# Kernel tuning notes

Hardware: AMD Instinct MI355X
Metric: run time of the kernel (lower is better)

Reference implementation:

```python
import jax, jax.numpy as jnp
import numpy as np


def setup_inputs() -> dict:
    key = jax.random.key(0)
    B, C, H, W = 8, 64, 64, 64
    x = jax.random.normal(key, (B, C, H, W), dtype=jnp.float32)
    return {"x": x}


def reference(x) -> jnp.ndarray:
    # x: (B, C, H, W). Spatial self-attention over N = H*W positions with
    # Q = K = V = flattened x, no scaling, no projections (the Conv2d in the
    # original __init__ is never used in forward).
    B, C, H, W = x.shape
    N = H * W
    f = x.reshape(B, C, N)  # (B, C, N)
    # att[b, n, m] = sum_c f[b, c, n] * f[b, c, m]  -> (B, N, N)
    att = jnp.einsum('bcn,bcm->bnm', f, f)
    att = jax.nn.softmax(att, axis=-1)
    # outp[b, c, n] = sum_m f[b, c, m] * att[b, n, m]^T  (f_x @ att)
    outp = jnp.einsum('bcm,bmn->bcn', f, att).reshape(B, C, H, W)
    return x + outp
```

## Files before the change

kernel.cpp:

```cpp
#include <hip/hip_runtime.h>

typedef short v8s __attribute__((ext_vector_type(8)));
typedef float v4f __attribute__((ext_vector_type(4)));

#define CC 64
#define NN 4096
#define NKT 32
#define LOG2E 1.44269504088896340736f

#define WS_FBF_T 0u
#define WS_FBF   4194304u
#define WS_G     8388608u
#define WS_MAXN  8519680u
#define WS_NEED  8519712u

__device__ __forceinline__ unsigned short f2bf_rne(float f) {
  unsigned int u = __builtin_bit_cast(unsigned int, f);
  u += 0x7FFFu + ((u >> 16) & 1u);
  return (unsigned short)(u >> 16);
}

__global__ __launch_bounds__(256) void prep_kernel(
    const float* __restrict__ x, unsigned short* __restrict__ fbf_t,
    unsigned short* __restrict__ fbf, float* __restrict__ g, int* __restrict__ maxn) {
  __shared__ unsigned short T[64 * 72];
  __shared__ float red[16][64];
  const int t = threadIdx.x;
  const int b = blockIdx.x & 7;
  const int n0 = (blockIdx.x >> 3) << 6;
  const int nn = (t & 15) << 2;
  float ps0 = 0.f, ps1 = 0.f, ps2 = 0.f, ps3 = 0.f;
#pragma unroll
  for (int j = 0; j < 4; ++j) {
    int c = (t >> 4) + j * 16;
    size_t gidx = ((size_t)(b * 64 + c) << 12) + (unsigned)(n0 + nn);
    float4 v = *(const float4*)(x + gidx);
    ushort4 w;
    w.x = f2bf_rne(v.x); w.y = f2bf_rne(v.y); w.z = f2bf_rne(v.z); w.w = f2bf_rne(v.w);
    *(ushort4*)(fbf + gidx) = w;
    T[(nn + 0) * 72 + c] = w.x;
    T[(nn + 1) * 72 + c] = w.y;
    T[(nn + 2) * 72 + c] = w.z;
    T[(nn + 3) * 72 + c] = w.w;
    ps0 += v.x * v.x; ps1 += v.y * v.y; ps2 += v.z * v.z; ps3 += v.w * v.w;
  }
  red[t >> 4][nn + 0] = ps0; red[t >> 4][nn + 1] = ps1;
  red[t >> 4][nn + 2] = ps2; red[t >> 4][nn + 3] = ps3;
  __syncthreads();
  if (t < 64) {
    float gs = 0.f;
#pragma unroll
    for (int i = 0; i < 16; ++i) gs += red[i][t];
    g[b * 4096 + n0 + t] = gs;
    float m = gs;
    m = fmaxf(m, __shfl_xor(m, 1, 64));
    m = fmaxf(m, __shfl_xor(m, 2, 64));
    m = fmaxf(m, __shfl_xor(m, 4, 64));
    m = fmaxf(m, __shfl_xor(m, 8, 64));
    m = fmaxf(m, __shfl_xor(m, 16, 64));
    m = fmaxf(m, __shfl_xor(m, 32, 64));
    if (t == 0) atomicMax(maxn + b, __float_as_int(m));
  }
#pragma unroll
  for (int i = 0; i < 2; ++i) {
    int idx = t + i * 256;
    int n = idx >> 3, cs = (idx & 7) << 3;
    *(v8s*)(fbf_t + (((size_t)b << 12) + (unsigned)(n0 + n)) * 64 + cs) =
        *(const v8s*)&T[n * 72 + cs];
  }
}

__global__ __launch_bounds__(512, 2) void chanattn_main(
    const float* __restrict__ x, const unsigned short* __restrict__ fbf_t,
    const unsigned short* __restrict__ fbf, const float* __restrict__ g,
    const int* __restrict__ maxn, float* __restrict__ out) {
  __shared__ __align__(16) unsigned char smem[56320];
  unsigned short* sKt = (unsigned short*)smem;
  unsigned short* sVc = (unsigned short*)(smem + 18432);
  unsigned short* sP  = (unsigned short*)(smem + 35840);

  const int tid = threadIdx.x;
  const int wave = tid >> 6, lane = tid & 63, quad = lane >> 4, l15 = lane & 15;
  const int qg = wave >> 2, kg = wave & 3;
  const int b = blockIdx.x & 7, qt = blockIdx.x >> 3;

  const unsigned short* fT = fbf_t + (((size_t)b << 12) << 6);
  const unsigned short* fV = fbf + ((size_t)b << 18);

  const int sKey = tid >> 3, sC = (tid & 7) << 3;
  const int vC = tid >> 4, vK = (tid & 15) << 3;

#pragma unroll
  for (int i = 0; i < 2; ++i) {
    int key = sKey + i * 64;
    *(v8s*)&sKt[key * 72 + sC] =
        *(const v8s*)&fT[((size_t)(qt * 128 + key)) * 64 + sC];
  }
  __syncthreads();
  v8s aqf[4][2];
#pragma unroll
  for (int mt = 0; mt < 4; ++mt)
#pragma unroll
    for (int cs = 0; cs < 2; ++cs)
      aqf[mt][cs] = *(const v8s*)&sKt[(qg * 64 + mt * 16 + l15) * 72 + cs * 32 + quad * 8];

  float msc[4][4];
  {
    const float gmax = __int_as_float(maxn[b]);
#pragma unroll
    for (int mt = 0; mt < 4; ++mt)
#pragma unroll
      for (int r = 0; r < 4; ++r) {
        int row = qt * 128 + qg * 64 + mt * 16 + quad * 4 + r;
        msc[mt][r] = __builtin_sqrtf(g[b * 4096 + row] * gmax) * LOG2E;
      }
  }
  __syncthreads();

  v8s pf[4];
#pragma unroll
  for (int i = 0; i < 2; ++i)
    pf[i] = *(const v8s*)&fT[((size_t)(sKey + i * 64)) * 64 + sC];
#pragma unroll
  for (int i = 0; i < 2; ++i)
    pf[2 + i] = *(const v8s*)&fV[(size_t)(vC + i * 32) * 4096 + vK];

  v4f oacc[4][4];
  float rsum[4][4];
#pragma unroll
  for (int mt = 0; mt < 4; ++mt)
#pragma unroll
    for (int r = 0; r < 4; ++r) {
      oacc[mt][r] = (v4f){0.f, 0.f, 0.f, 0.f};
      rsum[mt][r] = 0.f;
    }
  unsigned short* sPw = sP + wave * (32 * 40);

  for (int kt = 0; kt < NKT; ++kt) {
#pragma unroll
    for (int i = 0; i < 2; ++i)
      *(v8s*)&sKt[(sKey + i * 64) * 72 + sC] = pf[i];
#pragma unroll
    for (int i = 0; i < 2; ++i)
      *(v8s*)&sVc[(vC + i * 32) * 136 + vK] = pf[2 + i];
    __syncthreads();
    if (kt + 1 < NKT) {
      const int k0 = (kt + 1) * 128;
#pragma unroll
      for (int i = 0; i < 2; ++i)
        pf[i] = *(const v8s*)&fT[((size_t)(k0 + sKey + i * 64)) * 64 + sC];
#pragma unroll
      for (int i = 0; i < 2; ++i)
        pf[2 + i] = *(const v8s*)&fV[(size_t)(vC + i * 32) * 4096 + k0 + vK];
    }

    v4f sacc[4][2];
#pragma unroll
    for (int mt = 0; mt < 4; ++mt)
#pragma unroll
      for (int nt = 0; nt < 2; ++nt) sacc[mt][nt] = (v4f){0.f, 0.f, 0.f, 0.f};
#pragma unroll
    for (int nt = 0; nt < 2; ++nt)
#pragma unroll
      for (int cs = 0; cs < 2; ++cs) {
        v8s bK = *(const v8s*)&sKt[(kg * 32 + 2 * l15 + nt) * 72 + cs * 32 + quad * 8];
#pragma unroll
        for (int mt = 0; mt < 4; ++mt)
          sacc[mt][nt] =
              __builtin_amdgcn_mfma_f32_16x16x32_bf16(aqf[mt][cs], bK, sacc[mt][nt], 0, 0, 0);
      }

    unsigned int pk[4][4];
#pragma unroll
    for (int mt = 0; mt < 4; ++mt)
#pragma unroll
      for (int r = 0; r < 4; ++r) {
        float p0 = __builtin_amdgcn_exp2f(__builtin_fmaf(sacc[mt][0][r], LOG2E, -msc[mt][r]));
        float p1 = __builtin_amdgcn_exp2f(__builtin_fmaf(sacc[mt][1][r], LOG2E, -msc[mt][r]));
        rsum[mt][r] += p0 + p1;
        unsigned int u0 = __builtin_bit_cast(unsigned int, p0);
        unsigned int u1 = __builtin_bit_cast(unsigned int, p1);
        pk[mt][r] = (u1 & 0xFFFF0000u) | (u0 >> 16);
      }

    v8s bV[4];
#pragma unroll
    for (int ct = 0; ct < 4; ++ct)
      bV[ct] = *(const v8s*)&sVc[(ct * 16 + l15) * 136 + kg * 32 + quad * 8];
#pragma unroll
    for (int h = 0; h < 2; ++h) {
#pragma unroll
      for (int m2 = 0; m2 < 2; ++m2)
#pragma unroll
        for (int r = 0; r < 4; ++r)
          *(unsigned int*)&sPw[(m2 * 16 + quad * 4 + r) * 40 + 2 * l15] = pk[h * 2 + m2][r];
      asm volatile("s_waitcnt lgkmcnt(0)" ::: "memory");
      v8s aP[2];
#pragma unroll
      for (int m2 = 0; m2 < 2; ++m2)
        aP[m2] = *(const v8s*)&sPw[(m2 * 16 + l15) * 40 + quad * 8];
      asm volatile("s_waitcnt lgkmcnt(0)" ::: "memory");
#pragma unroll
      for (int m2 = 0; m2 < 2; ++m2)
#pragma unroll
        for (int ct = 0; ct < 4; ++ct)
          oacc[h * 2 + m2][ct] = __builtin_amdgcn_mfma_f32_16x16x32_bf16(
              aP[m2], bV[ct], oacc[h * 2 + m2][ct], 0, 0, 0);
    }
    __syncthreads();
  }

#pragma unroll
  for (int mt = 0; mt < 4; ++mt)
#pragma unroll
    for (int r = 0; r < 4; ++r) {
      float s = rsum[mt][r];
      s += __shfl_xor(s, 1, 64);
      s += __shfl_xor(s, 2, 64);
      s += __shfl_xor(s, 4, 64);
      s += __shfl_xor(s, 8, 64);
      rsum[mt][r] = s;
    }
  float* lred = (float*)(smem + 35840);
  if (l15 == 0) {
#pragma unroll
    for (int mt = 0; mt < 4; ++mt)
#pragma unroll
      for (int r = 0; r < 4; ++r)
        lred[(qg * 64 + mt * 16 + quad * 4 + r) * 4 + kg] = rsum[mt][r];
  }
  __syncthreads();
  float inv[4][4];
#pragma unroll
  for (int mt = 0; mt < 4; ++mt)
#pragma unroll
    for (int r = 0; r < 4; ++r) {
      const float4 lv = *(const float4*)&lred[(qg * 64 + mt * 16 + quad * 4 + r) * 4];
      inv[mt][r] = __builtin_amdgcn_rcpf(lv.x + lv.y + lv.z + lv.w);
    }

  float* Obuf = (float*)smem;
#pragma unroll
  for (int round = 0; round < 4; ++round) {
    if (kg == round) {
#pragma unroll
      for (int mt = 0; mt < 4; ++mt)
#pragma unroll
        for (int ct = 0; ct < 4; ++ct)
#pragma unroll
          for (int r = 0; r < 4; ++r) {
            float val = oacc[mt][ct][r] * inv[mt][r];
            float* p = &Obuf[(qg * 64 + ct * 16 + l15) * 68 + mt * 16 + quad * 4 + r];
            if (round == 0) *p = val; else *p += val;
          }
    }
    __syncthreads();
  }
#pragma unroll
  for (int j = 0; j < 4; ++j) {
    int idx = tid + j * 512;
    int qg2 = idx >> 10, c = (idx >> 4) & 63, q4 = idx & 15;
    const float4 o = *(const float4*)&Obuf[(qg2 * 64 + c) * 68 + q4 * 4];
    size_t gidx = ((size_t)(b * 64 + c) << 12) + (unsigned)(qt * 128 + qg2 * 64 + q4 * 4);
    const float4 xv = *(const float4*)(x + gidx);
    float4 rv;
    rv.x = xv.x + o.x; rv.y = xv.y + o.y; rv.z = xv.z + o.z; rv.w = xv.w + o.w;
    *(float4*)(out + gidx) = rv;
  }
}

__global__ __launch_bounds__(512) void
chanattn_fallback(const float* __restrict__ x, float* __restrict__ out) {
  __shared__ __align__(16) unsigned char smem[54272];
  unsigned short* sKt = (unsigned short*)smem;
  unsigned short* sVc = (unsigned short*)(smem + 18432);
  unsigned short* sP  = (unsigned short*)(smem + 35840);
  const int tid = threadIdx.x;
  const int wave = tid >> 6, lane = tid & 63, quad = lane >> 4, l15 = lane & 15;
  const int b = blockIdx.x & 7, qt = blockIdx.x >> 3;
  const float* fb = x + (size_t)b * (CC * NN);
  const int skey = tid & 127, sc0 = (tid >> 7) << 4;
  {
    float vq[16];
#pragma unroll
    for (int j = 0; j < 16; ++j) vq[j] = fb[(sc0 + j) * NN + qt * 128 + skey];
    unsigned short us[16];
#pragma unroll
    for (int j = 0; j < 16; ++j) us[j] = f2bf_rne(vq[j]);
#pragma unroll
    for (int h = 0; h < 2; ++h) {
      v8s t;
#pragma unroll
      for (int j = 0; j < 8; ++j) t[j] = (short)us[h * 8 + j];
      *(v8s*)&sKt[skey * 72 + sc0 + h * 8] = t;
    }
  }
  float vk[16];
#pragma unroll
  for (int j = 0; j < 16; ++j) vk[j] = fb[(sc0 + j) * NN + skey];
  __syncthreads();
  v8s aq[2];
#pragma unroll
  for (int cs = 0; cs < 2; ++cs)
    aq[cs] = *(const v8s*)&sKt[(wave * 16 + l15) * 72 + cs * 32 + quad * 8];
  __syncthreads();
  v4f oacc[4];
#pragma unroll
  for (int ct = 0; ct < 4; ++ct) oacc[ct] = (v4f){0.f, 0.f, 0.f, 0.f};
  float m_run[4], l_run[4];
#pragma unroll
  for (int r = 0; r < 4; ++r) { m_run[r] = -3.0e38f; l_run[r] = 0.f; }
  unsigned short* sPw = sP + wave * (16 * 72);
  for (int kt = 0; kt < 32; ++kt) {
    {
      unsigned short us[16];
#pragma unroll
      for (int j = 0; j < 16; ++j) us[j] = f2bf_rne(vk[j]);
#pragma unroll
      for (int h = 0; h < 2; ++h) {
        v8s t;
#pragma unroll
        for (int j = 0; j < 8; ++j) t[j] = (short)us[h * 8 + j];
        *(v8s*)&sKt[skey * 72 + sc0 + h * 8] = t;
      }
#pragma unroll
      for (int j = 0; j < 16; ++j) sVc[(sc0 + j) * 136 + skey] = us[j];
    }
    __syncthreads();
    if (kt + 1 < 32) {
      const int m0 = (kt + 1) * 128;
#pragma unroll
      for (int j = 0; j < 16; ++j) vk[j] = fb[(sc0 + j) * NN + m0 + skey];
    }
    v4f sacc[8];
#pragma unroll
    for (int t = 0; t < 8; ++t) {
      v4f acc = (v4f){0.f, 0.f, 0.f, 0.f};
#pragma unroll
      for (int cs = 0; cs < 2; ++cs) {
        v8s bf = *(const v8s*)&sKt[(t * 16 + l15) * 72 + cs * 32 + quad * 8];
        acc = __builtin_amdgcn_mfma_f32_16x16x32_bf16(aq[cs], bf, acc, 0, 0, 0);
      }
      sacc[t] = acc;
    }
    float alpha[4], msc[4], rsum[4];
#pragma unroll
    for (int r = 0; r < 4; ++r) {
      float mv = sacc[0][r];
#pragma unroll
      for (int t = 1; t < 8; ++t) mv = fmaxf(mv, sacc[t][r]);
      mv = fmaxf(mv, __shfl_xor(mv, 8, 64));
      mv = fmaxf(mv, __shfl_xor(mv, 4, 64));
      mv = fmaxf(mv, __shfl_xor(mv, 2, 64));
      mv = fmaxf(mv, __shfl_xor(mv, 1, 64));
      float mnew = fmaxf(m_run[r], mv);
      alpha[r] = __builtin_amdgcn_exp2f((m_run[r] - mnew) * LOG2E);
      m_run[r] = mnew;
      msc[r] = mnew * LOG2E;
      l_run[r] *= alpha[r];
      rsum[r] = 0.f;
    }
#pragma unroll
    for (int ct = 0; ct < 4; ++ct)
#pragma unroll
      for (int r = 0; r < 4; ++r) oacc[ct][r] *= alpha[r];
#pragma unroll
    for (int half = 0; half < 2; ++half) {
#pragma unroll
      for (int t = half * 4; t < half * 4 + 4; ++t)
#pragma unroll
        for (int r = 0; r < 4; ++r) {
          float p = __builtin_amdgcn_exp2f(__builtin_fmaf(sacc[t][r], LOG2E, -msc[r]));
          rsum[r] += p;
          sPw[(quad * 4 + r) * 72 + (t - half * 4) * 16 + l15] = f2bf_rne(p);
        }
      asm volatile("s_waitcnt lgkmcnt(0)" ::: "memory");
#pragma unroll
      for (int ms = 0; ms < 2; ++ms) {
        v8s af = *(const v8s*)&sPw[l15 * 72 + ms * 32 + quad * 8];
#pragma unroll
        for (int ct = 0; ct < 4; ++ct) {
          v8s bf = *(const v8s*)&sVc[(ct * 16 + l15) * 136 + (half * 2 + ms) * 32 + quad * 8];
          oacc[ct] = __builtin_amdgcn_mfma_f32_16x16x32_bf16(af, bf, oacc[ct], 0, 0, 0);
        }
      }
      asm volatile("s_waitcnt lgkmcnt(0)" ::: "memory");
    }
#pragma unroll
    for (int r = 0; r < 4; ++r) {
      float s = rsum[r];
      s += __shfl_xor(s, 8, 64);
      s += __shfl_xor(s, 4, 64);
      s += __shfl_xor(s, 2, 64);
      s += __shfl_xor(s, 1, 64);
      l_run[r] += s;
    }
    __syncthreads();
  }
  float inv[4];
#pragma unroll
  for (int r = 0; r < 4; ++r) inv[r] = __builtin_amdgcn_rcpf(l_run[r]);
  float* sOt = (float*)smem;
#pragma unroll
  for (int ct = 0; ct < 4; ++ct)
#pragma unroll
    for (int r = 0; r < 4; ++r)
      sOt[(ct * 16 + l15) * 132 + wave * 16 + quad * 4 + r] = oacc[ct][r] * inv[r];
  __syncthreads();
#pragma unroll
  for (int j = 0; j < 4; ++j) {
    int idx = tid + j * 512;
    int nv = idx & 31, c = idx >> 5;
    float4 o = *(const float4*)&sOt[c * 132 + nv * 4];
    size_t gaddr = (size_t)b * (CC * NN) + (size_t)c * NN + (size_t)(qt * 128 + nv * 4);
    float4 xv = *(const float4*)(x + gaddr);
    float4 res = make_float4(xv.x + o.x, xv.y + o.y, xv.z + o.z, xv.w + o.w);
    *(float4*)(out + gaddr) = res;
  }
}

extern "C" void kernel_launch(void* const* d_in, const int* in_sizes, int n_in,
                              void* d_out, int out_size, void* d_ws, size_t ws_size,
                              hipStream_t stream) {
  const float* xin = (const float*)d_in[0];
  float* out = (float*)d_out;
  if (ws_size >= (size_t)WS_NEED) {
    unsigned short* fbf_t = (unsigned short*)((char*)d_ws + WS_FBF_T);
    unsigned short* fbf = (unsigned short*)((char*)d_ws + WS_FBF);
    float* g = (float*)((char*)d_ws + WS_G);
    int* maxn = (int*)((char*)d_ws + WS_MAXN);
    hipMemsetAsync(maxn, 0, 8 * sizeof(int), stream);
    prep_kernel<<<dim3(512), dim3(256), 0, stream>>>(xin, fbf_t, fbf, g, maxn);
    chanattn_main<<<dim3(256), dim3(512), 0, stream>>>(xin, fbf_t, fbf, g, maxn, out);
  } else {
    chanattn_fallback<<<dim3(256), dim3(512), 0, stream>>>(xin, out);
  }
}
```

Baseline: 120.7 us.

## Transpose attention MFMAs so P stays in registers, drop LDS P roundtrip

The score MFMA is reordered to compute S^T (keys as rows, queries as columns), so each lane's exp outputs can be packed directly into the B operand of the PV MFMA with no per-wave LDS staging buffer for P. V is stored in LDS with a permuted column slot so its fragment order matches the register-packed P layout. The K/V tile loop now reads its fragments into registers before a barrier and then writes the next tile, which double-buffers through registers and frees shared memory. This removes LDS writes and reads plus waitcnt stalls per tile, but adds a second barrier per iteration and depends on the permuted-slot mapping being correct.

```diff
diff --git a/kernel.cpp b/kernel.cpp
--- a/kernel.cpp
+++ b/kernel.cpp
@@ -1,11 +1,9 @@
 #include <hip/hip_runtime.h>
 
 typedef short v8s __attribute__((ext_vector_type(8)));
+typedef short v4s __attribute__((ext_vector_type(4)));
 typedef float v4f __attribute__((ext_vector_type(4)));
 
-#define CC 64
-#define NN 4096
-#define NKT 32
 #define LOG2E 1.44269504088896340736f
 
 #define WS_FBF_T 0u
@@ -74,183 +72,183 @@
     const float* __restrict__ x, const unsigned short* __restrict__ fbf_t,
     const unsigned short* __restrict__ fbf, const float* __restrict__ g,
     const int* __restrict__ maxn, float* __restrict__ out) {
-  __shared__ __align__(16) unsigned char smem[56320];
+  __shared__ __align__(16) unsigned char smem[37888];
   unsigned short* sKt = (unsigned short*)smem;
   unsigned short* sVc = (unsigned short*)(smem + 18432);
-  unsigned short* sP  = (unsigned short*)(smem + 35840);
+  float* lred = (float*)(smem + 35840);
 
   const int tid = threadIdx.x;
   const int wave = tid >> 6, lane = tid & 63, quad = lane >> 4, l15 = lane & 15;
   const int qg = wave >> 2, kg = wave & 3;
   const int b = blockIdx.x & 7, qt = blockIdx.x >> 3;
 
-  const unsigned short* fT = fbf_t + (((size_t)b << 12) << 6);
+  const unsigned short* fT = fbf_t + ((size_t)b << 18);
   const unsigned short* fV = fbf + ((size_t)b << 18);
 
   const int sKey = tid >> 3, sC = (tid & 7) << 3;
   const int vC = tid >> 4, vK = (tid & 15) << 3;
-
-#pragma unroll
-  for (int i = 0; i < 2; ++i) {
-    int key = sKey + i * 64;
-    *(v8s*)&sKt[key * 72 + sC] =
-        *(const v8s*)&fT[((size_t)(qt * 128 + key)) * 64 + sC];
-  }
-  __syncthreads();
-  v8s aqf[4][2];
-#pragma unroll
-  for (int mt = 0; mt < 4; ++mt)
+  const int vSlot = (vK & ~31) + ((vK & 8) ? 16 : 0) + ((vK & 16) ? 4 : 0);
+
+#pragma unroll
+  for (int i = 0; i < 2; ++i)
+    *(v8s*)&sKt[(sKey + i * 64) * 72 + sC] =
+        *(const v8s*)&fT[(size_t)(qt * 128 + sKey + i * 64) * 64 + sC];
+
+  v8s pfk[2], pfv[2];
+#pragma unroll
+  for (int i = 0; i < 2; ++i)
+    pfk[i] = *(const v8s*)&fT[(size_t)(sKey + i * 64) * 64 + sC];
+#pragma unroll
+  for (int i = 0; i < 2; ++i)
+    pfv[i] = *(const v8s*)&fV[(size_t)(vC + i * 32) * 4096 + vK];
+
+  __syncthreads();
+  v8s bQ[4][2];
+#pragma unroll
+  for (int jq = 0; jq < 4; ++jq)
 #pragma unroll
     for (int cs = 0; cs < 2; ++cs)
-      aqf[mt][cs] = *(const v8s*)&sKt[(qg * 64 + mt * 16 + l15) * 72 + cs * 32 + quad * 8];
-
-  float msc[4][4];
+      bQ[jq][cs] = *(const v8s*)&sKt[(qg * 64 + jq * 16 + l15) * 72 + cs * 32 + quad * 8];
+
+  float msc[4];
   {
     const float gmax = __int_as_float(maxn[b]);
 #pragma unroll
-    for (int mt = 0; mt < 4; ++mt)
+    for (int jq = 0; jq < 4; ++jq) {
+      int row = qt * 128 + qg * 64 + jq * 16 + l15;
+      msc[jq] = __builtin_sqrtf(g[b * 4096 + row] * gmax) * LOG2E;
+    }
+  }
+  __syncthreads();
+
+#pragma unroll
+  for (int i = 0; i < 2; ++i)
+    *(v8s*)&sKt[(sKey + i * 64) * 72 + sC] = pfk[i];
+#pragma unroll
+  for (int i = 0; i < 2; ++i) {
+    v4s lo, hi;
+#pragma unroll
+    for (int j = 0; j < 4; ++j) { lo[j] = pfv[i][j]; hi[j] = pfv[i][j + 4]; }
+    *(v4s*)&sVc[(vC + i * 32) * 136 + vSlot] = lo;
+    *(v4s*)&sVc[(vC + i * 32) * 136 + vSlot + 8] = hi;
+  }
+
+  v4f oacc[4][4];
+  float rsum[4];
+#pragma unroll
+  for (int ct = 0; ct < 4; ++ct)
+#pragma unroll
+    for (int jq = 0; jq < 4; ++jq) oacc[ct][jq] = (v4f){0.f, 0.f, 0.f, 0.f};
+#pragma unroll
+  for (int jq = 0; jq < 4; ++jq) rsum[jq] = 0.f;
+
+  for (int kt = 0; kt < 32; ++kt) {
+    __syncthreads();
+
+    if (kt + 1 < 32) {
+      const int k0 = (kt + 1) * 128;
+#pragma unroll
+      for (int i = 0; i < 2; ++i)
+        pfk[i] = *(const v8s*)&fT[(size_t)(k0 + sKey + i * 64) * 64 + sC];
+#pragma unroll
+      for (int i = 0; i < 2; ++i)
+        pfv[i] = *(const v8s*)&fV[(size_t)(vC + i * 32) * 4096 + k0 + vK];
+    }
+
+    v8s aK[2][2];
+#pragma unroll
+    for (int t = 0; t < 2; ++t)
+#pragma unroll
+      for (int cs = 0; cs < 2; ++cs)
+        aK[t][cs] =
+            *(const v8s*)&sKt[(kg * 32 + t * 16 + l15) * 72 + cs * 32 + quad * 8];
+    v8s aV[4];
+#pragma unroll
+    for (int ct = 0; ct < 4; ++ct)
+      aV[ct] = *(const v8s*)&sVc[(ct * 16 + l15) * 136 + kg * 32 + quad * 8];
+
+    __syncthreads();
+
+    if (kt + 1 < 32) {
+#pragma unroll
+      for (int i = 0; i < 2; ++i)
+        *(v8s*)&sKt[(sKey + i * 64) * 72 + sC] = pfk[i];
+#pragma unroll
+      for (int i = 0; i < 2; ++i) {
+        v4s lo, hi;
+#pragma unroll
+        for (int j = 0; j < 4; ++j) { lo[j] = pfv[i][j]; hi[j] = pfv[i][j + 4]; }
+        *(v4s*)&sVc[(vC + i * 32) * 136 + vSlot] = lo;
+        *(v4s*)&sVc[(vC + i * 32) * 136 + vSlot + 8] = hi;
+      }
+    }
+
+#pragma unroll
+    for (int jq = 0; jq < 4; ++jq) {
+      v4f s0 = (v4f){0.f, 0.f, 0.f, 0.f};
+      v4f s1 = (v4f){0.f, 0.f, 0.f, 0.f};
+#pragma unroll
+      for (int cs = 0; cs < 2; ++cs) {
+        s0 = __builtin_amdgcn_mfma_f32_16x16x32_bf16(aK[0][cs], bQ[jq][cs], s0, 0, 0, 0);
+        s1 = __builtin_amdgcn_mfma_f32_16x16x32_bf16(aK[1][cs], bQ[jq][cs], s1, 0, 0, 0);
+      }
+      float p0[4], p1[4];
 #pragma unroll
       for (int r = 0; r < 4; ++r) {
-        int row = qt * 128 + qg * 64 + mt * 16 + quad * 4 + r;
-        msc[mt][r] = __builtin_sqrtf(g[b * 4096 + row] * gmax) * LOG2E;
-      }
-  }
-  __syncthreads();
-
-  v8s pf[4];
-#pragma unroll
-  for (int i = 0; i < 2; ++i)
-    pf[i] = *(const v8s*)&fT[((size_t)(sKey + i * 64)) * 64 + sC];
-#pragma unroll
-  for (int i = 0; i < 2; ++i)
-    pf[2 + i] = *(const v8s*)&fV[(size_t)(vC + i * 32) * 4096 + vK];
-
-  v4f oacc[4][4];
-  float rsum[4][4];
-#pragma unroll
-  for (int mt = 0; mt < 4; ++mt)
-#pragma unroll
-    for (int r = 0; r < 4; ++r) {
-      oacc[mt][r] = (v4f){0.f, 0.f, 0.f, 0.f};
-      rsum[mt][r] = 0.f;
-    }
-  unsigned short* sPw = sP + wave * (32 * 40);
-
-  for (int kt = 0; kt < NKT; ++kt) {
-#pragma unroll
-    for (int i = 0; i < 2; ++i)
-      *(v8s*)&sKt[(sKey + i * 64) * 72 + sC] = pf[i];
-#pragma unroll
-    for (int i = 0; i < 2; ++i)
-      *(v8s*)&sVc[(vC + i * 32) * 136 + vK] = pf[2 + i];
-    __syncthreads();
-    if (kt + 1 < NKT) {
-      const int k0 = (kt + 1) * 128;
-#pragma unroll
-      for (int i = 0; i < 2; ++i)
-        pf[i] = *(const v8s*)&fT[((size_t)(k0 + sKey + i * 64)) * 64 + sC];
-#pragma unroll
-      for (int i = 0; i < 2; ++i)
-        pf[2 + i] = *(const v8s*)&fV[(size_t)(vC + i * 32) * 4096 + k0 + vK];
-    }
-
-    v4f sacc[4][2];
-#pragma unroll
-    for (int mt = 0; mt < 4; ++mt)
-#pragma unroll
-      for (int nt = 0; nt < 2; ++nt) sacc[mt][nt] = (v4f){0.f, 0.f, 0.f, 0.f};
-#pragma unroll
-    for (int nt = 0; nt < 2; ++nt)
-#pragma unroll
-      for (int cs = 0; cs < 2; ++cs) {
-        v8s bK = *(const v8s*)&sKt[(kg * 32 + 2 * l15 + nt) * 72 + cs * 32 + quad * 8];
-#pragma unroll
-        for (int mt = 0; mt < 4; ++mt)
-          sacc[mt][nt] =
-              __builtin_amdgcn_mfma_f32_16x16x32_bf16(aqf[mt][cs], bK, sacc[mt][nt], 0, 0, 0);
-      }
-
-    unsigned int pk[4][4];
-#pragma unroll
-    for (int mt = 0; mt < 4; ++mt)
-#pragma unroll
-      for (int r = 0; r < 4; ++r) {
-        float p0 = __builtin_amdgcn_exp2f(__builtin_fmaf(sacc[mt][0][r], LOG2E, -msc[mt][r]));
-        float p1 = __builtin_amdgcn_exp2f(__builtin_fmaf(sacc[mt][1][r], LOG2E, -msc[mt][r]));
-        rsum[mt][r] += p0 + p1;
-        unsigned int u0 = __builtin_bit_cast(unsigned int, p0);
-        unsigned int u1 = __builtin_bit_cast(unsigned int, p1);
-        pk[mt][r] = (u1 & 0xFFFF0000u) | (u0 >> 16);
-      }
-
-    v8s bV[4];
-#pragma unroll
-    for (int ct = 0; ct < 4; ++ct)
-      bV[ct] = *(const v8s*)&sVc[(ct * 16 + l15) * 136 + kg * 32 + quad * 8];
-#pragma unroll
-    for (int h = 0; h < 2; ++h) {
-#pragma unroll
-      for (int m2 = 0; m2 < 2; ++m2)
-#pragma unroll
-        for (int r = 0; r < 4; ++r)
-          *(unsigned int*)&sPw[(m2 * 16 + quad * 4 + r) * 40 + 2 * l15] = pk[h * 2 + m2][r];
-      asm volatile("s_waitcnt lgkmcnt(0)" ::: "memory");
-      v8s aP[2];
-#pragma unroll
-      for (int m2 = 0; m2 < 2; ++m2)
-        aP[m2] = *(const v8s*)&sPw[(m2 * 16 + l15) * 40 + quad * 8];
-      asm volatile("s_waitcnt lgkmcnt(0)" ::: "memory");
-#pragma unroll
-      for (int m2 = 0; m2 < 2; ++m2)
-#pragma unroll
-        for (int ct = 0; ct < 4; ++ct)
-          oacc[h * 2 + m2][ct] = __builtin_amdgcn_mfma_f32_16x16x32_bf16(
-              aP[m2], bV[ct], oacc[h * 2 + m2][ct], 0, 0, 0);
-    }
-    __syncthreads();
-  }
-
-#pragma unroll
-  for (int mt = 0; mt < 4; ++mt)
-#pragma unroll
-    for (int r = 0; r < 4; ++r) {
-      float s = rsum[mt][r];
-      s += __shfl_xor(s, 1, 64);
-      s += __shfl_xor(s, 2, 64);
-      s += __shfl_xor(s, 4, 64);
-      s += __shfl_xor(s, 8, 64);
-      rsum[mt][r] = s;
-    }
-  float* lred = (float*)(smem + 35840);
-  if (l15 == 0) {
-#pragma unroll
-    for (int mt = 0; mt < 4; ++mt)
-#pragma unroll
-      for (int r = 0; r < 4; ++r)
-        lred[(qg * 64 + mt * 16 + quad * 4 + r) * 4 + kg] = rsum[mt][r];
-  }
-  __syncthreads();
-  float inv[4][4];
-#pragma unroll
-  for (int mt = 0; mt < 4; ++mt)
-#pragma unroll
-    for (int r = 0; r < 4; ++r) {
-      const float4 lv = *(const float4*)&lred[(qg * 64 + mt * 16 + quad * 4 + r) * 4];
-      inv[mt][r] = __builtin_amdgcn_rcpf(lv.x + lv.y + lv.z + lv.w);
-    }
+        p0[r] = __builtin_amdgcn_exp2f(__builtin_fmaf(s0[r], LOG2E, -msc[jq]));
+        p1[r] = __builtin_amdgcn_exp2f(__builtin_fmaf(s1[r], LOG2E, -msc[jq]));
+      }
+      rsum[jq] += ((p0[0] + p0[1]) + (p0[2] + p0[3])) +
+                  ((p1[0] + p1[1]) + (p1[2] + p1[3]));
+      uint4 up;
+      up.x = (__builtin_bit_cast(unsigned int, p0[1]) & 0xFFFF0000u) |
+             (__builtin_bit_cast(unsigned int, p0[0]) >> 16);
+      up.y = (__builtin_bit_cast(unsigned int, p0[3]) & 0xFFFF0000u) |
+             (__builtin_bit_cast(unsigned int, p0[2]) >> 16);
+      up.z = (__builtin_bit_cast(unsigned int, p1[1]) & 0xFFFF0000u) |
+             (__builtin_bit_cast(unsigned int, p1[0]) >> 16);
+      up.w = (__builtin_bit_cast(unsigned int, p1[3]) & 0xFFFF0000u) |
+             (__builtin_bit_cast(unsigned int, p1[2]) >> 16);
+      v8s bp = __builtin_bit_cast(v8s, up);
+#pragma unroll
+      for (int ct = 0; ct < 4; ++ct)
+        oacc[ct][jq] =
+            __builtin_amdgcn_mfma_f32_16x16x32_bf16(aV[ct], bp, oacc[ct][jq], 0, 0, 0);
+    }
+  }
+
+#pragma unroll
+  for (int jq = 0; jq < 4; ++jq) {
+    float s = rsum[jq];
+    s += __shfl_xor(s, 16, 64);
+    s += __shfl_xor(s, 32, 64);
+    rsum[jq] = s;
+  }
+  if (quad == 0) {
+#pragma unroll
+    for (int jq = 0; jq < 4; ++jq)
+      lred[(qg * 64 + jq * 16 + l15) * 4 + kg] = rsum[jq];
+  }
+  __syncthreads();
+  float inv[4];
+#pragma unroll
+  for (int jq = 0; jq < 4; ++jq) {
+    const float4 lv = *(const float4*)&lred[(qg * 64 + jq * 16 + l15) * 4];
+    inv[jq] = __builtin_amdgcn_rcpf((lv.x + lv.y) + (lv.z + lv.w));
+  }
 
   float* Obuf = (float*)smem;
 #pragma unroll
   for (int round = 0; round < 4; ++round) {
     if (kg == round) {
 #pragma unroll
-      for (int mt = 0; mt < 4; ++mt)
-#pragma unroll
-        for (int ct = 0; ct < 4; ++ct)
+      for (int ct = 0; ct < 4; ++ct)
+#pragma unroll
+        for (int jq = 0; jq < 4; ++jq)
 #pragma unroll
           for (int r = 0; r < 4; ++r) {
-            float val = oacc[mt][ct][r] * inv[mt][r];
-            float* p = &Obuf[(qg * 64 + ct * 16 + l15) * 68 + mt * 16 + quad * 4 + r];
+            float val = oacc[ct][jq][r] * inv[jq];
+            float* p = &Obuf[(qg * 64 + ct * 16 + quad * 4 + r) * 68 + jq * 16 + l15];
             if (round == 0) *p = val; else *p += val;
           }
     }
@@ -278,12 +276,12 @@
   const int tid = threadIdx.x;
   const int wave = tid >> 6, lane = tid & 63, quad = lane >> 4, l15 = lane & 15;
   const int b = blockIdx.x & 7, qt = blockIdx.x >> 3;
-  const float* fb = x + (size_t)b * (CC * NN);
+  const float* fb = x + (size_t)b * (64 * 4096);
   const int skey = tid & 127, sc0 = (tid >> 7) << 4;
   {
     float vq[16];
 #pragma unroll
-    for (int j = 0; j < 16; ++j) vq[j] = fb[(sc0 + j) * NN + qt * 128 + skey];
+    for (int j = 0; j < 16; ++j) vq[j] = fb[(sc0 + j) * 4096 + qt * 128 + skey];
     unsigned short us[16];
 #pragma unroll
     for (int j = 0; j < 16; ++j) us[j] = f2bf_rne(vq[j]);
@@ -297,7 +295,7 @@
   }
   float vk[16];
 #pragma unroll
-  for (int j = 0; j < 16; ++j) vk[j] = fb[(sc0 + j) * NN + skey];
+  for (int j = 0; j < 16; ++j) vk[j] = fb[(sc0 + j) * 4096 + skey];
   __syncthreads();
   v8s aq[2];
 #pragma unroll
@@ -330,7 +328,7 @@
     if (kt + 1 < 32) {
       const int m0 = (kt + 1) * 128;
 #pragma unroll
-      for (int j = 0; j < 16; ++j) vk[j] = fb[(sc0 + j) * NN + m0 + skey];
+      for (int j = 0; j < 16; ++j) vk[j] = fb[(sc0 + j) * 4096 + m0 + skey];
     }
     v4f sacc[8];
 #pragma unroll
@@ -412,7 +410,7 @@
     int idx = tid + j * 512;
     int nv = idx & 31, c = idx >> 5;
     float4 o = *(const float4*)&sOt[c * 132 + nv * 4];
-    size_t gaddr = (size_t)b * (CC * NN) + (size_t)c * NN + (size_t)(qt * 128 + nv * 4);
+    size_t gaddr = (size_t)b * (64 * 4096) + (size_t)c * 4096 + (size_t)(qt * 128 + nv * 4);
     float4 xv = *(const float4*)(x + gaddr);
     float4 res = make_float4(xv.x + o.x, xv.y + o.y, xv.z + o.z, xv.w + o.w);
     *(float4*)(out + gaddr) = res;
```

Result: faster. 118.2 us (-2.1%).
